# Kernel optimization log

Measured on AMD Instinct MI355X. Metric: run time of the kernel, lower is better.

Reference implementation:

```python
import jax, jax.numpy as jnp
import numpy as np

B, S, D_IN, D = 2, 4096, 1024, 64  # batch, seq_len, input_dim, head dim d


def setup_inputs() -> dict:
    key = jax.random.key(0)
    k1, k2, k3, k4 = jax.random.split(key, 4)
    X = jax.random.normal(k1, (B, S, D_IN), dtype=jnp.float32)
    W_q = jax.random.normal(k2, (D_IN, 2 * D), dtype=jnp.float32) / np.sqrt(D_IN)
    W_k = jax.random.normal(k3, (D_IN, 2 * D), dtype=jnp.float32) / np.sqrt(D_IN)
    W_v = jax.random.normal(k4, (D_IN, 2 * D), dtype=jnp.float32) / np.sqrt(D_IN)
    lam = jnp.float32(0.8)
    return {"X": X, "W_q": W_q, "W_k": W_k, "W_v": W_v, "lam": lam}


def reference(X, W_q, W_k, W_v, lam):
    d = W_q.shape[-1] // 2
    Q = X @ W_q  # [B, S, 2d]
    K = X @ W_k  # [B, S, 2d]
    V = X @ W_v  # [B, S, 2d]
    Q1, Q2 = Q[..., :d], Q[..., d:]
    K1, K2 = K[..., :d], K[..., d:]
    s = 1.0 / jnp.sqrt(jnp.float32(d))
    A1 = jnp.einsum("bqd,bkd->bqk", Q1, K1) * s  # [B, S, S]
    A2 = jnp.einsum("bqd,bkd->bqk", Q2, K2) * s  # [B, S, S]
    P = jax.nn.softmax(A1, axis=-1) - lam * jax.nn.softmax(A2, axis=-1)
    return jnp.einsum("bqk,bkv->bqv", P, V)  # [B, S, 2d]
```

## Files before the change

### kernel.cpp

```cpp
#include <hip/hip_runtime.h>
#include <hip/hip_bf16.h>

typedef float f32x4 __attribute__((ext_vector_type(4)));
typedef float f32x16 __attribute__((ext_vector_type(16)));
typedef short bf16x8 __attribute__((ext_vector_type(8)));

#define MFMA16(A,B,C) __builtin_amdgcn_mfma_f32_16x16x32_bf16(A,B,C,0,0,0)
#define MFMA32(A,B,C) __builtin_amdgcn_mfma_f32_32x32x16_bf16(A,B,C,0,0,0)

__device__ __forceinline__ unsigned short f2bf(float f) {
    union { float f; unsigned u; } x; x.f = f;
    return (unsigned short)((x.u + 0x7FFFu + ((x.u >> 16) & 1u)) >> 16);
}

__device__ __forceinline__ float bf2f(unsigned short u) {
    union { unsigned u; float f; } x; x.u = ((unsigned)u) << 16; return x.f;
}

__device__ __forceinline__ unsigned fbits(float f) {
    union { float f; unsigned u; } x; x.f = f; return x.u;
}

__device__ __forceinline__ f32x16 zero16() {
    f32x16 z;
#pragma unroll
    for (int i = 0; i < 16; ++i) z[i] = 0.f;
    return z;
}

typedef const __attribute__((address_space(1))) unsigned int* as1_t;
typedef __attribute__((address_space(3))) unsigned int* as3_t;
__device__ __forceinline__ void gl_lds16(const unsigned short* g, unsigned short* l) {
    __builtin_amdgcn_global_load_lds((as1_t)g, (as3_t)l, 16, 0, 0);
}

__global__ __launch_bounds__(256) void prep(const float* __restrict__ Wq,
        const float* __restrict__ Wk, const float* __restrict__ Wv,
        const float* __restrict__ X, unsigned short* __restrict__ WT,
        unsigned short* __restrict__ Xb) {
    if (blockIdx.x < 96) {
        int w = blockIdx.x % 3;
        int kt = blockIdx.x / 3;
        const float* src = (w == 0) ? Wq : (w == 1) ? Wk : Wv;
        int k0 = kt * 32;
#pragma unroll
        for (int j = 0; j < 16; ++j) {
            int idx = threadIdx.x + j * 256;
            int r = idx >> 7, c = idx & 127;
            float v = src[(size_t)(k0 + r) * 128 + c];
            WT[(size_t)(w * 128 + c) * 1024 + k0 + r] = f2bf(v);
        }
    } else {
        int i = (blockIdx.x - 96) * 256 + threadIdx.x;
#pragma unroll
        for (int r = 0; r < 8; ++r) {
            int idx = i + r * 262144;
            float4 x = ((const float4*)X)[idx];
            ushort4 p;
            p.x = f2bf(x.x); p.y = f2bf(x.y); p.z = f2bf(x.z); p.w = f2bf(x.w);
            ((ushort4*)Xb)[idx] = p;
        }
    }
}

__global__ __launch_bounds__(256) void proj(const unsigned short* __restrict__ Xb,
        const unsigned short* __restrict__ WT, unsigned short* __restrict__ Qc,
        unsigned short* __restrict__ Kc, unsigned short* __restrict__ VT) {
    int tid = threadIdx.x;
    int w = tid >> 6, lane = tid & 63;
    int lr = lane & 15, lg = lane >> 4;
    int wr = w >> 1, wc = w & 1;
    int m0 = blockIdx.x * 64;
    int n0 = blockIdx.y * 96;

    __shared__ __align__(16) unsigned short Ab[3][64 * 64];
    __shared__ __align__(16) unsigned short Bb[3][96 * 64];

    f32x4 acc[2][3];
#pragma unroll
    for (int i = 0; i < 2; ++i)
#pragma unroll
        for (int j = 0; j < 3; ++j) acc[i][j] = f32x4{0.f,0.f,0.f,0.f};

    int srow = lane >> 3;
    int sunit = lane & 7;
    const unsigned short* aSrc = Xb + (size_t)(m0 + srow) * 1024 + sunit * 8;
    const unsigned short* bSrc = WT + (size_t)(n0 + srow) * 1024 + sunit * 8;

    auto STAGE = [&](unsigned short* ad, unsigned short* bd, int st) {
        int kk = st * 64;
#pragma unroll
        for (int i = 0; i < 2; ++i) {
            int blk = w * 2 + i;
            gl_lds16(aSrc + (size_t)blk * 8 * 1024 + kk, ad + blk * 512);
        }
#pragma unroll
        for (int i = 0; i < 3; ++i) {
            int blk = w * 3 + i;
            gl_lds16(bSrc + (size_t)blk * 8 * 1024 + kk, bd + blk * 512);
        }
    };

    unsigned short *a0 = Ab[0], *a1 = Ab[1], *a2 = Ab[2];
    unsigned short *b0 = Bb[0], *b1 = Bb[1], *b2 = Bb[2];
    STAGE(a0, b0, 0);
    STAGE(a1, b1, 1);

    for (int st = 0; st < 16; ++st) {
        if (st < 15) asm volatile("s_waitcnt vmcnt(5)" ::: "memory");
        else         asm volatile("s_waitcnt vmcnt(0)" ::: "memory");
        __builtin_amdgcn_sched_barrier(0);
        __builtin_amdgcn_s_barrier();
        __builtin_amdgcn_sched_barrier(0);
        if (st + 2 < 16) STAGE(a2, b2, st + 2);

        const unsigned short* ab = a0;
        const unsigned short* bb = b0;
#pragma unroll
        for (int ksub = 0; ksub < 2; ++ksub) {
            int ko = ksub * 32 + lg * 8;
            bf16x8 af[2], bf[3];
#pragma unroll
            for (int mt = 0; mt < 2; ++mt)
                af[mt] = *(const bf16x8*)(ab + (wr * 32 + mt * 16 + lr) * 64 + ko);
#pragma unroll
            for (int nt = 0; nt < 3; ++nt)
                bf[nt] = *(const bf16x8*)(bb + (wc * 48 + nt * 16 + lr) * 64 + ko);
#pragma unroll
            for (int mt = 0; mt < 2; ++mt)
#pragma unroll
                for (int nt = 0; nt < 3; ++nt)
                    acc[mt][nt] = MFMA16(af[mt], bf[nt], acc[mt][nt]);
        }
        unsigned short* t;
        t = a0; a0 = a1; a1 = a2; a2 = t;
        t = b0; b0 = b1; b1 = b2; b2 = t;
    }

    int b = m0 >> 12;
    int sbase = (m0 & 4095) + wr * 32;
#pragma unroll
    for (int nt = 0; nt < 3; ++nt) {
        int gcol = n0 + wc * 48 + nt * 16 + lr;
        int tensor = gcol >> 7;
#pragma unroll
        for (int mt = 0; mt < 2; ++mt) {
            int sloc = sbase + mt * 16 + 4 * lg;
            if (tensor == 2) {
                int vcol = gcol & 127;
                int slocV = (sloc & ~15) | (((lg & 1) << 3) | ((lg >> 1) << 2));
                ushort4 pk;
                pk.x = f2bf(acc[mt][nt][0]); pk.y = f2bf(acc[mt][nt][1]);
                pk.z = f2bf(acc[mt][nt][2]); pk.w = f2bf(acc[mt][nt][3]);
                *(ushort4*)(VT + (size_t)(b * 128 + vcol) * 4096 + slocV) = pk;
            } else {
                int within = gcol & 127;
                int comp = within >> 6;
                int col64 = within & 63;
                float sc = (tensor == 0) ? 0.1803368801f : 1.0f;
                unsigned short* dst = (tensor == 0) ? Qc : Kc;
                size_t rowb = (size_t)(comp * 2 + b) * 4096 + sloc;
#pragma unroll
                for (int r = 0; r < 4; ++r)
                    dst[(rowb + r) * 64 + col64] = f2bf(acc[mt][nt][r] * sc);
            }
        }
    }
}

__global__ __launch_bounds__(256, 2) void attn(const unsigned short* __restrict__ Qc,
        const unsigned short* __restrict__ Kc, const unsigned short* __restrict__ VT,
        unsigned short* __restrict__ Opart, float* __restrict__ Lpart) {
    int tid = threadIdx.x;
    int wave = tid >> 6, lane = tid & 63;
    int l31 = lane & 31, hi = lane >> 5;
    int x7 = l31 & 7;
    int b = blockIdx.y;
    int comp = blockIdx.z >> 2, split = blockIdx.z & 3;
    int q0 = blockIdx.x * 128 + wave * 32;
    int kstart = split * 1024;

    __shared__ __align__(16) unsigned short kb3[3][64 * 64];
    __shared__ __align__(16) unsigned short vb3[3][128 * 64];

    const unsigned short* Qp = Qc + ((size_t)(comp * 2 + b) * 4096 + q0 + l31) * 64 + hi * 8;
    bf16x8 qB0 = *(const bf16x8*)(Qp);
    bf16x8 qB1 = *(const bf16x8*)(Qp + 16);
    bf16x8 qB2 = *(const bf16x8*)(Qp + 32);
    bf16x8 qB3 = *(const bf16x8*)(Qp + 48);

    f32x16 o[4];
#pragma unroll
    for (int i = 0; i < 4; ++i) o[i] = zero16();
    float lsum = 0.f;

    const unsigned short* kSrc = Kc + ((size_t)(comp * 2 + b) * 4096 + kstart
                                       + wave * 8 + (lane >> 3)) * 64
                                    + ((lane & 7) ^ (lane >> 3)) * 8;
    const unsigned short* vSrc = VT + ((size_t)b * 128 + (tid >> 3)) * 4096
                                    + kstart + ((lane & 7) ^ (lane >> 3)) * 8;

    auto STAGE = [&](unsigned short* kd, unsigned short* vd, int it) {
        const unsigned short* ks = kSrc + (size_t)it * 4096;
        gl_lds16(ks,        kd + wave * 512);
        gl_lds16(ks + 2048, kd + 2048 + wave * 512);
        const unsigned short* vs = vSrc + it * 64;
#pragma unroll
        for (int ri = 0; ri < 4; ++ri)
            gl_lds16(vs + (size_t)ri * 32 * 4096, vd + ri * 2048 + wave * 512);
    };

    unsigned short *k0 = kb3[0], *k1 = kb3[1], *k2 = kb3[2];
    unsigned short *v0 = vb3[0], *v1 = vb3[1], *v2 = vb3[2];
    STAGE(k0, v0, 0);
    STAGE(k1, v1, 1);

    for (int it = 0; it < 16; ++it) {
        if (it < 15) asm volatile("s_waitcnt vmcnt(6)" ::: "memory");
        else         asm volatile("s_waitcnt vmcnt(0)" ::: "memory");
        __builtin_amdgcn_sched_barrier(0);
        __builtin_amdgcn_s_barrier();
        __builtin_amdgcn_sched_barrier(0);
        if (it + 2 < 16) STAGE(k2, v2, it + 2);

        const unsigned short* kb = k0;
        const unsigned short* vb = v0;

        f32x16 st0 = zero16(), st1 = zero16();
        __builtin_amdgcn_s_setprio(1);
#pragma unroll
        for (int j = 0; j < 4; ++j) {
            int ku = ((j * 2 + hi) ^ x7) * 8;
            bf16x8 kA0 = *(const bf16x8*)(kb + l31 * 64 + ku);
            bf16x8 kA1 = *(const bf16x8*)(kb + (32 + l31) * 64 + ku);
            bf16x8 qj = (j == 0) ? qB0 : (j == 1) ? qB1 : (j == 2) ? qB2 : qB3;
            st0 = MFMA32(kA0, qj, st0);
            st1 = MFMA32(kA1, qj, st1);
        }
        __builtin_amdgcn_s_setprio(0);

        union W4 { unsigned u[4]; bf16x8 v; };
        W4 wA0, wB0, wA1, wB1;
#pragma unroll
        for (int i2 = 0; i2 < 4; ++i2) {
            float a0 = __builtin_amdgcn_exp2f(st0[2 * i2]);
            float a1 = __builtin_amdgcn_exp2f(st0[2 * i2 + 1]);
            float a2 = __builtin_amdgcn_exp2f(st0[8 + 2 * i2]);
            float a3 = __builtin_amdgcn_exp2f(st0[9 + 2 * i2]);
            float b0 = __builtin_amdgcn_exp2f(st1[2 * i2]);
            float b1 = __builtin_amdgcn_exp2f(st1[2 * i2 + 1]);
            float b2 = __builtin_amdgcn_exp2f(st1[8 + 2 * i2]);
            float b3 = __builtin_amdgcn_exp2f(st1[9 + 2 * i2]);
            lsum += (a0 + a1) + (a2 + a3) + (b0 + b1) + (b2 + b3);
            wA0.u[i2] = __builtin_amdgcn_perm(fbits(a1), fbits(a0), 0x07060302);
            wB0.u[i2] = __builtin_amdgcn_perm(fbits(a3), fbits(a2), 0x07060302);
            wA1.u[i2] = __builtin_amdgcn_perm(fbits(b1), fbits(b0), 0x07060302);
            wB1.u[i2] = __builtin_amdgcn_perm(fbits(b3), fbits(b2), 0x07060302);
        }

        __builtin_amdgcn_s_setprio(1);
#pragma unroll
        for (int vt = 0; vt < 4; ++vt) {
            const unsigned short* vrow = vb + (vt * 32 + l31) * 64;
            o[vt] = MFMA32(wA0.v, *(const bf16x8*)(vrow + ((0 + hi) ^ x7) * 8), o[vt]);
            o[vt] = MFMA32(wB0.v, *(const bf16x8*)(vrow + ((2 + hi) ^ x7) * 8), o[vt]);
            o[vt] = MFMA32(wA1.v, *(const bf16x8*)(vrow + ((4 + hi) ^ x7) * 8), o[vt]);
            o[vt] = MFMA32(wB1.v, *(const bf16x8*)(vrow + ((6 + hi) ^ x7) * 8), o[vt]);
        }
        __builtin_amdgcn_s_setprio(0);

        unsigned short* t;
        t = k0; k0 = k1; k1 = k2; k2 = t;
        t = v0; v0 = v1; v1 = v2; v2 = t;
    }

    int base = (b * 2 + comp) * 4 + split;
    unsigned short* op = Opart + (size_t)base * 4096 * 128;
#pragma unroll
    for (int vt = 0; vt < 4; ++vt)
#pragma unroll
        for (int r = 0; r < 16; ++r) {
            int qr = (r & 3) + 8 * (r >> 2) + 4 * hi;
            op[(size_t)(q0 + qr) * 128 + vt * 32 + l31] = f2bf(o[vt][r]);
        }
    float ls = lsum + __shfl_xor(lsum, 32, 64);
    if (hi == 0)
        Lpart[(size_t)base * 4096 + q0 + l31] = ls;
}

__global__ __launch_bounds__(256) void combine(const unsigned short* __restrict__ Opart,
        const float* __restrict__ Lpart, const float* __restrict__ lamp,
        float* __restrict__ out) {
    float lam = lamp[0];
    int i = blockIdx.x * 256 + threadIdx.x;
    int row = i >> 5;
    int c4  = i & 31;
    int b = row >> 12, q = row & 4095;

    float l1 = 0.f, l2 = 0.f;
#pragma unroll
    for (int s = 0; s < 4; ++s) {
        l1 += Lpart[((size_t)((b * 2 + 0) * 4 + s)) * 4096 + q];
        l2 += Lpart[((size_t)((b * 2 + 1) * 4 + s)) * 4096 + q];
    }
    float rl1 = 1.0f / l1, rl2 = 1.0f / l2;

    size_t qoff = (size_t)q * 128 + c4 * 4;
    float a0 = 0.f, a1 = 0.f, a2 = 0.f, a3 = 0.f;
    float c0 = 0.f, c1 = 0.f, c2 = 0.f, c3 = 0.f;
#pragma unroll
    for (int s = 0; s < 4; ++s) {
        ushort4 p1 = *(const ushort4*)(Opart + (size_t)((b * 2 + 0) * 4 + s) * 4096 * 128 + qoff);
        ushort4 p2 = *(const ushort4*)(Opart + (size_t)((b * 2 + 1) * 4 + s) * 4096 * 128 + qoff);
        a0 += bf2f(p1.x); a1 += bf2f(p1.y); a2 += bf2f(p1.z); a3 += bf2f(p1.w);
        c0 += bf2f(p2.x); c1 += bf2f(p2.y); c2 += bf2f(p2.z); c3 += bf2f(p2.w);
    }
    float4 r;
    r.x = a0 * rl1 - lam * c0 * rl2;
    r.y = a1 * rl1 - lam * c1 * rl2;
    r.z = a2 * rl1 - lam * c2 * rl2;
    r.w = a3 * rl1 - lam * c3 * rl2;
    ((float4*)out)[i] = r;
}

extern "C" void kernel_launch(void* const* d_in, const int* in_sizes, int n_in,
                              void* d_out, int out_size, void* d_ws, size_t ws_size,
                              hipStream_t stream) {
    const float* X   = (const float*)d_in[0];
    const float* Wq  = (const float*)d_in[1];
    const float* Wk  = (const float*)d_in[2];
    const float* Wv  = (const float*)d_in[3];
    const float* lam = (const float*)d_in[4];
    float* out = (float*)d_out;

    char* ws = (char*)d_ws;
    unsigned short* Qc = (unsigned short*)(ws);
    unsigned short* Kc = (unsigned short*)(ws + 2097152);
    unsigned short* VT = (unsigned short*)(ws + 4194304);
    unsigned short* WT = (unsigned short*)(ws + 6291456);
    unsigned short* Xb = (unsigned short*)(ws + 7077888);
    unsigned short* Opart = (unsigned short*)(ws + 6291456);
    float* Lpart = (float*)(ws + 23068672);

    prep<<<dim3(1120), dim3(256), 0, stream>>>(Wq, Wk, Wv, X, WT, Xb);
    proj<<<dim3(128, 4), dim3(256), 0, stream>>>(Xb, WT, Qc, Kc, VT);
    attn<<<dim3(32, 2, 8), dim3(256), 0, stream>>>(Qc, Kc, VT, Opart, Lpart);
    combine<<<dim3(1024), dim3(256), 0, stream>>>(Opart, Lpart, lam, out);
}
```

Measured before the change: 70.59 us.

## Fuse X bf16 conversion into projection GEMM via register-staged A loads

```diff
diff --git a/kernel.cpp b/kernel.cpp
--- a/kernel.cpp
+++ b/kernel.cpp
@@ -36,34 +36,21 @@
 
 __global__ __launch_bounds__(256) void prep(const float* __restrict__ Wq,
         const float* __restrict__ Wk, const float* __restrict__ Wv,
-        const float* __restrict__ X, unsigned short* __restrict__ WT,
-        unsigned short* __restrict__ Xb) {
-    if (blockIdx.x < 96) {
-        int w = blockIdx.x % 3;
-        int kt = blockIdx.x / 3;
-        const float* src = (w == 0) ? Wq : (w == 1) ? Wk : Wv;
-        int k0 = kt * 32;
-#pragma unroll
-        for (int j = 0; j < 16; ++j) {
-            int idx = threadIdx.x + j * 256;
-            int r = idx >> 7, c = idx & 127;
-            float v = src[(size_t)(k0 + r) * 128 + c];
-            WT[(size_t)(w * 128 + c) * 1024 + k0 + r] = f2bf(v);
-        }
-    } else {
-        int i = (blockIdx.x - 96) * 256 + threadIdx.x;
-#pragma unroll
-        for (int r = 0; r < 8; ++r) {
-            int idx = i + r * 262144;
-            float4 x = ((const float4*)X)[idx];
-            ushort4 p;
-            p.x = f2bf(x.x); p.y = f2bf(x.y); p.z = f2bf(x.z); p.w = f2bf(x.w);
-            ((ushort4*)Xb)[idx] = p;
-        }
-    }
-}
-
-__global__ __launch_bounds__(256) void proj(const unsigned short* __restrict__ Xb,
+        unsigned short* __restrict__ WT) {
+    int w = blockIdx.x % 3;
+    int kt = blockIdx.x / 3;
+    const float* src = (w == 0) ? Wq : (w == 1) ? Wk : Wv;
+    int k0 = kt * 32;
+#pragma unroll
+    for (int j = 0; j < 16; ++j) {
+        int idx = threadIdx.x + j * 256;
+        int r = idx >> 7, c = idx & 127;
+        float v = src[(size_t)(k0 + r) * 128 + c];
+        WT[(size_t)(w * 128 + c) * 1024 + k0 + r] = f2bf(v);
+    }
+}
+
+__global__ __launch_bounds__(256) void proj(const float* __restrict__ Xf,
         const unsigned short* __restrict__ WT, unsigned short* __restrict__ Qc,
         unsigned short* __restrict__ Kc, unsigned short* __restrict__ VT) {
     int tid = threadIdx.x;
@@ -84,16 +71,31 @@
 
     int srow = lane >> 3;
     int sunit = lane & 7;
-    const unsigned short* aSrc = Xb + (size_t)(m0 + srow) * 1024 + sunit * 8;
     const unsigned short* bSrc = WT + (size_t)(n0 + srow) * 1024 + sunit * 8;
 
-    auto STAGE = [&](unsigned short* ad, unsigned short* bd, int st) {
+    float4 aReg[4];
+    auto A_LOAD = [&](int st) {
         int kk = st * 64;
 #pragma unroll
-        for (int i = 0; i < 2; ++i) {
-            int blk = w * 2 + i;
-            gl_lds16(aSrc + (size_t)blk * 8 * 1024 + kk, ad + blk * 512);
-        }
+        for (int i = 0; i < 4; ++i) {
+            int f = tid + i * 256;
+            int row = f >> 4, c4 = f & 15;
+            aReg[i] = *(const float4*)(Xf + (size_t)(m0 + row) * 1024 + kk + c4 * 4);
+        }
+    };
+    auto A_WRITE = [&](unsigned short* ad) {
+#pragma unroll
+        for (int i = 0; i < 4; ++i) {
+            int f = tid + i * 256;
+            int row = f >> 4, c4 = f & 15;
+            ushort4 pk;
+            pk.x = f2bf(aReg[i].x); pk.y = f2bf(aReg[i].y);
+            pk.z = f2bf(aReg[i].z); pk.w = f2bf(aReg[i].w);
+            *(ushort4*)(ad + row * 64 + c4 * 4) = pk;
+        }
+    };
+    auto B_STAGE = [&](unsigned short* bd, int st) {
+        int kk = st * 64;
 #pragma unroll
         for (int i = 0; i < 3; ++i) {
             int blk = w * 3 + i;
@@ -103,16 +105,18 @@
 
     unsigned short *a0 = Ab[0], *a1 = Ab[1], *a2 = Ab[2];
     unsigned short *b0 = Bb[0], *b1 = Bb[1], *b2 = Bb[2];
-    STAGE(a0, b0, 0);
-    STAGE(a1, b1, 1);
+    A_LOAD(0); B_STAGE(b0, 0);
+    A_WRITE(a0);
+    A_LOAD(1); B_STAGE(b1, 1);
+    A_WRITE(a1);
 
     for (int st = 0; st < 16; ++st) {
-        if (st < 15) asm volatile("s_waitcnt vmcnt(5)" ::: "memory");
-        else         asm volatile("s_waitcnt vmcnt(0)" ::: "memory");
+        if (st < 15) asm volatile("s_waitcnt vmcnt(3) lgkmcnt(0)" ::: "memory");
+        else         asm volatile("s_waitcnt vmcnt(0) lgkmcnt(0)" ::: "memory");
         __builtin_amdgcn_sched_barrier(0);
         __builtin_amdgcn_s_barrier();
         __builtin_amdgcn_sched_barrier(0);
-        if (st + 2 < 16) STAGE(a2, b2, st + 2);
+        if (st + 2 < 16) { A_LOAD(st + 2); B_STAGE(b2, st + 2); }
 
         const unsigned short* ab = a0;
         const unsigned short* bb = b0;
@@ -132,6 +136,8 @@
                 for (int nt = 0; nt < 3; ++nt)
                     acc[mt][nt] = MFMA16(af[mt], bf[nt], acc[mt][nt]);
         }
+        if (st + 2 < 16) A_WRITE(a2);
+
         unsigned short* t;
         t = a0; a0 = a1; a1 = a2; a2 = t;
         t = b0; b0 = b1; b1 = b2; b2 = t;
@@ -338,12 +344,11 @@
     unsigned short* Kc = (unsigned short*)(ws + 2097152);
     unsigned short* VT = (unsigned short*)(ws + 4194304);
     unsigned short* WT = (unsigned short*)(ws + 6291456);
-    unsigned short* Xb = (unsigned short*)(ws + 7077888);
     unsigned short* Opart = (unsigned short*)(ws + 6291456);
     float* Lpart = (float*)(ws + 23068672);
 
-    prep<<<dim3(1120), dim3(256), 0, stream>>>(Wq, Wk, Wv, X, WT, Xb);
-    proj<<<dim3(128, 4), dim3(256), 0, stream>>>(Xb, WT, Qc, Kc, VT);
+    prep<<<dim3(96), dim3(256), 0, stream>>>(Wq, Wk, Wv, WT);
+    proj<<<dim3(128, 4), dim3(256), 0, stream>>>(X, WT, Qc, Kc, VT);
     attn<<<dim3(32, 2, 8), dim3(256), 0, stream>>>(Qc, Kc, VT, Opart, Lpart);
     combine<<<dim3(1024), dim3(256), 0, stream>>>(Opart, Lpart, lam, out);
 }
```

Result: faster. 66.84 us, median of 3 (-5.3%).
